# Kernel tuning notes

Hardware: AMD Instinct MI355X
Metric: run time of the kernel (lower is better)

The kernel has to match this reference:

```python
import jax, jax.numpy as jnp
import numpy as np

N_NODES = 100000
N_EDGES = 3200000
IN_CH = 256
OUT_CH = 128


def setup_inputs() -> dict:
    key = jax.random.key(0)
    k1, k2, k3, k4, k5 = jax.random.split(key, 5)
    x = jax.random.normal(k1, (N_NODES, IN_CH), dtype=jnp.float32)
    edge_src = jax.random.randint(k2, (N_EDGES,), 0, N_NODES, dtype=jnp.int64 if jax.config.jax_enable_x64 else jnp.int32)
    edge_dst = jax.random.randint(k3, (N_EDGES,), 0, N_NODES, dtype=jnp.int64 if jax.config.jax_enable_x64 else jnp.int32)
    edge_vals = jax.random.uniform(k4, (N_EDGES,), dtype=jnp.float32)
    weight = jax.random.normal(k5, (IN_CH, OUT_CH), dtype=jnp.float32) * (2.0 / (IN_CH + OUT_CH)) ** 0.5  # glorot
    bias = jnp.zeros((OUT_CH,), dtype=jnp.float32)
    return {"x": x, "edge_src": edge_src, "edge_dst": edge_dst,
            "edge_vals": edge_vals, "weight": weight, "bias": bias}


def reference(x, edge_src, edge_dst, edge_vals, weight, bias):
    # out = A @ (x @ W) + b, with A given in COO form (edge_src=row, edge_dst=col, edge_vals)
    xw = x @ weight                                  # [N, out]
    msgs = xw[edge_dst] * edge_vals[:, None]         # gather source features, scale by edge weight
    agg = jax.ops.segment_sum(msgs, edge_src, num_segments=N_NODES)  # scatter-add to rows
    return agg + bias
```

## Files before the change

kernel.cpp:

```cpp
#include <hip/hip_runtime.h>

#define N_NODES 100000
#define N_EDGES 3200000
#define IN_CH   256
#define OUT_CH  128

#define BSH        5
#define BN         32
#define NBIN       3125
#define NBLK1      256
#define EPB1       12500
#define ITER1      4
#define NS1        (NBIN * NBLK1)
#define SCAN_CHUNK 8192
#define NBLK_S1    ((NS1 + SCAN_CHUNK - 1) / SCAN_CHUNK)
#define SCAP       2048

#define OFF_XWB    0
#define OFF_WBF    25600000
#define OFF_CNTT   25665536
#define OFF_CNTA   28865536
#define OFF_RPA    32065536
#define OFF_RPT    35265552
#define OFF_BS     38465552
#define OFF_RPN    38466576
#define OFF_PACKED 38866592

typedef __attribute__((ext_vector_type(8))) short    bf8;
typedef __attribute__((ext_vector_type(4))) float    f4;
typedef __attribute__((ext_vector_type(4))) unsigned uv4;
typedef __attribute__((ext_vector_type(2))) float    f2v;

__device__ __forceinline__ unsigned f2bf(float f) {
    unsigned u = __float_as_uint(f);
    return (u + 0x7fffu + ((u >> 16) & 1u)) >> 16;
}

__device__ __forceinline__ unsigned cvt_pk_bf16(float lo, float hi) {
    unsigned r;
    asm("v_cvt_pk_bf16_f32 %0, %1, %2" : "=v"(r) : "v"(lo), "v"(hi));
    return r;
}

__global__ __launch_bounds__(256) void wcvt_kernel(const float* __restrict__ w,
                                                   unsigned short* __restrict__ wbf) {
    int t = threadIdx.x;
    int k = blockIdx.x * 2 + (t >> 7);
    int n = t & 127;
    wbf[n * 256 + k] = (unsigned short)f2bf(w[k * 128 + n]);
}

__global__ __launch_bounds__(256) void gemm_kernel(const float* __restrict__ x,
                                                   const unsigned short* __restrict__ wbf,
                                                   unsigned* __restrict__ xwb) {
    int wave = threadIdx.x >> 6;
    int lane = threadIdx.x & 63;
    int m = lane & 15;
    int q = lane >> 4;
    int r0 = blockIdx.x * 64 + wave * 16;

    int arow = r0 + m;
    if (arow >= N_NODES) arow = N_NODES - 1;
    const float* xr = x + (long long)arow * IN_CH + q * 8;

    f4 acc[8];
#pragma unroll
    for (int ct = 0; ct < 8; ++ct) acc[ct] = (f4){0.f, 0.f, 0.f, 0.f};

#pragma unroll
    for (int ks = 0; ks < 8; ++ks) {
        float4 xa = *(const float4*)(xr + ks * 32);
        float4 xb = *(const float4*)(xr + ks * 32 + 4);
        uv4 au;
        au[0] = cvt_pk_bf16(xa.x, xa.y);
        au[1] = cvt_pk_bf16(xa.z, xa.w);
        au[2] = cvt_pk_bf16(xb.x, xb.y);
        au[3] = cvt_pk_bf16(xb.z, xb.w);
        bf8 a = __builtin_bit_cast(bf8, au);
#pragma unroll
        for (int ct = 0; ct < 8; ++ct) {
            uv4 u = *(const uv4*)&wbf[(ct * 16 + m) * 256 + ks * 32 + q * 8];
            bf8 b = __builtin_bit_cast(bf8, u);
            acc[ct] = __builtin_amdgcn_mfma_f32_16x16x32_bf16(a, b, acc[ct], 0, 0, 0);
        }
    }

#pragma unroll
    for (int ct = 0; ct < 8; ++ct) {
#pragma unroll
        for (int r = 0; r < 4; ++r) {
            float v = acc[ct][r];
            float p = __shfl_xor(v, 1, 64);
            unsigned wpk = cvt_pk_bf16(v, p);
            if (!(m & 1)) {
                int row = r0 + q * 4 + r;
                if (row < N_NODES)
                    xwb[row * 64 + ct * 8 + (m >> 1)] = wpk;
            }
        }
    }
}

__global__ __launch_bounds__(1024) void h1_kernel(const int* __restrict__ src,
                                                  int* __restrict__ cntT) {
    __shared__ int lc[NBIN];
    int tid = threadIdx.x;
    int bend = blockIdx.x * EPB1 + EPB1;
    for (int i = tid; i < NBIN; i += 1024) lc[i] = 0;
    __syncthreads();
#pragma unroll
    for (int k = 0; k < ITER1; ++k) {
        int i = blockIdx.x * EPB1 + k * 4096 + tid * 4;
        if (i < bend) {
            int4 s = *(const int4*)&src[i];
            atomicAdd(&lc[s.x >> BSH], 1);
            atomicAdd(&lc[s.y >> BSH], 1);
            atomicAdd(&lc[s.z >> BSH], 1);
            atomicAdd(&lc[s.w >> BSH], 1);
        }
    }
    __syncthreads();
    for (int i = tid; i < NBIN; i += 1024)
        cntT[blockIdx.x * NBIN + i] = lc[i];
}

__global__ __launch_bounds__(256) void transpose_kernel(const int* __restrict__ in,
                                                        int* __restrict__ out,
                                                        int R, int C) {
    __shared__ int t[32][33];
    int tx = threadIdx.x & 31, ty0 = threadIdx.x >> 5;
    int c0 = blockIdx.x * 32, r0 = blockIdx.y * 32;
#pragma unroll
    for (int i = 0; i < 4; ++i) {
        int r = r0 + ty0 + i * 8, c = c0 + tx;
        t[ty0 + i * 8][tx] = (r < R && c < C) ? in[r * C + c] : 0;
    }
    __syncthreads();
#pragma unroll
    for (int i = 0; i < 4; ++i) {
        int c = c0 + ty0 + i * 8, r = r0 + tx;
        if (c < C && r < R) out[c * R + r] = t[tx][ty0 + i * 8];
    }
}

__global__ __launch_bounds__(256) void scan_s1(const int* __restrict__ cnt,
                                               int* __restrict__ bsum) {
    __shared__ int wsum[4];
    int tid = threadIdx.x, lane = tid & 63, wid = tid >> 6;
    int acc = 0;
#pragma unroll
    for (int k = 0; k < SCAN_CHUNK / 1024; ++k) {
        int i0 = blockIdx.x * SCAN_CHUNK + k * 1024 + tid * 4;
        if (i0 < NS1) {
            int4 v = *(const int4*)&cnt[i0];
            acc += v.x + v.y + v.z + v.w;
        }
    }
#pragma unroll
    for (int off = 32; off; off >>= 1) acc += __shfl_down(acc, off, 64);
    if (lane == 0) wsum[wid] = acc;
    __syncthreads();
    if (tid == 0) bsum[blockIdx.x] = wsum[0] + wsum[1] + wsum[2] + wsum[3];
}

__global__ __launch_bounds__(256) void scan_s2(int* __restrict__ bsum,
                                               int* __restrict__ rpA,
                                               int* __restrict__ rpn) {
    __shared__ int wsum[4];
    int tid = threadIdx.x, lane = tid & 63, wid = tid >> 6;
    int v = (tid < NBLK_S1) ? bsum[tid] : 0;
    int s = v;
#pragma unroll
    for (int off = 1; off < 64; off <<= 1) {
        int t = __shfl_up(s, off, 64);
        if (lane >= off) s += t;
    }
    if (lane == 63) wsum[wid] = s;
    __syncthreads();
    int w0 = wsum[0], w1 = wsum[1], w2 = wsum[2], w3 = wsum[3];
    int woff = (wid > 0 ? w0 : 0) + (wid > 1 ? w1 : 0) + (wid > 2 ? w2 : 0);
    if (tid < NBLK_S1) bsum[tid] = woff + s - v;
    if (tid == 0) {
        int tot = w0 + w1 + w2 + w3;
        rpA[NS1] = tot;
        rpn[N_NODES] = tot;
    }
}

__global__ __launch_bounds__(256) void scan_s3(const int* __restrict__ cnt,
                                               const int* __restrict__ bsum,
                                               int* __restrict__ rpA) {
    __shared__ int wsum[4];
    int tid = threadIdx.x, lane = tid & 63, wid = tid >> 6;
    int carry = bsum[blockIdx.x];
#pragma unroll
    for (int k = 0; k < SCAN_CHUNK / 1024; ++k) {
        int i0 = blockIdx.x * SCAN_CHUNK + k * 1024 + tid * 4;
        int4 v = make_int4(0, 0, 0, 0);
        if (i0 < NS1) v = *(const int4*)&cnt[i0];
        int sum4 = v.x + v.y + v.z + v.w;
        int s = sum4;
#pragma unroll
        for (int off = 1; off < 64; off <<= 1) {
            int t = __shfl_up(s, off, 64);
            if (lane >= off) s += t;
        }
        if (lane == 63) wsum[wid] = s;
        __syncthreads();
        int w0 = wsum[0], w1 = wsum[1], w2 = wsum[2], w3 = wsum[3];
        int woff = (wid > 0 ? w0 : 0) + (wid > 1 ? w1 : 0) + (wid > 2 ? w2 : 0);
        int excl = carry + woff + (s - sum4);
        if (i0 < NS1)
            *(int4*)&rpA[i0] = make_int4(excl, excl + v.x, excl + v.x + v.y,
                                         excl + v.x + v.y + v.z);
        carry += w0 + w1 + w2 + w3;
        __syncthreads();
    }
}

__global__ __launch_bounds__(1024) void b1_kernel(const int* __restrict__ src,
                                                  const int* __restrict__ dst,
                                                  const float* __restrict__ val,
                                                  const int* __restrict__ rpT,
                                                  int2* __restrict__ p1) {
    __shared__ int lcur[NBIN];
    int tid = threadIdx.x;
    int bend = blockIdx.x * EPB1 + EPB1;
    for (int i = tid; i < NBIN; i += 1024)
        lcur[i] = rpT[blockIdx.x * NBIN + i];
    __syncthreads();
#pragma unroll
    for (int k = 0; k < ITER1; ++k) {
        int i = blockIdx.x * EPB1 + k * 4096 + tid * 4;
        if (i < bend) {
            int4   s = *(const int4*)&src[i];
            int4   d = *(const int4*)&dst[i];
            float4 v = *(const float4*)&val[i];
            int p;
            p = atomicAdd(&lcur[s.x >> BSH], 1);
            p1[p] = make_int2(d.x | ((s.x & (BN - 1)) << 17), __float_as_int(v.x));
            p = atomicAdd(&lcur[s.y >> BSH], 1);
            p1[p] = make_int2(d.y | ((s.y & (BN - 1)) << 17), __float_as_int(v.y));
            p = atomicAdd(&lcur[s.z >> BSH], 1);
            p1[p] = make_int2(d.z | ((s.z & (BN - 1)) << 17), __float_as_int(v.z));
            p = atomicAdd(&lcur[s.w >> BSH], 1);
            p1[p] = make_int2(d.w | ((s.w & (BN - 1)) << 17), __float_as_int(v.w));
        }
    }
}

__global__ __launch_bounds__(256) void sortf_kernel(const int2* __restrict__ p1,
                                                    const int* __restrict__ rpA,
                                                    int2* __restrict__ packed,
                                                    int* __restrict__ rpn) {
    __shared__ int  lcnt[BN];
    __shared__ int  lcur[BN];
    __shared__ int2 sbuf[SCAP];
    int b = blockIdx.x, tid = threadIdx.x;
    int beg = rpA[b * NBLK1];
    int end = rpA[(b + 1) * NBLK1];
    int n = end - beg;

    if (tid < BN) lcnt[tid] = 0;
    __syncthreads();

    if (n <= SCAP) {
        for (int e = tid; e < n; e += 256) {
            int2 q = p1[beg + e];
            sbuf[e] = q;
            atomicAdd(&lcnt[(q.x >> 17) & (BN - 1)], 1);
        }
    } else {
        for (int e = beg + tid; e < end; e += 256)
            atomicAdd(&lcnt[(p1[e].x >> 17) & (BN - 1)], 1);
    }
    __syncthreads();

    if (tid < BN) {
        int c = lcnt[tid];
        int v = c;
#pragma unroll
        for (int off = 1; off < BN; off <<= 1) {
            int t = __shfl_up(v, off, 64);
            if (tid >= off) v += t;
        }
        int excl = beg + v - c;
        lcur[tid] = excl;
        rpn[b * BN + tid] = excl;
    }
    __syncthreads();

    if (n <= SCAP) {
        for (int e = tid; e < n; e += 256) {
            int2 q = sbuf[e];
            int p = atomicAdd(&lcur[(q.x >> 17) & (BN - 1)], 1);
            packed[p] = make_int2(q.x & 0x1FFFF, q.y);
        }
    } else {
        for (int e = beg + tid; e < end; e += 256) {
            int2 q = p1[e];
            int p = atomicAdd(&lcur[(q.x >> 17) & (BN - 1)], 1);
            packed[p] = make_int2(q.x & 0x1FFFF, q.y);
        }
    }
}

__global__ __launch_bounds__(256) void aggregate_kernel(const int* __restrict__ rp,
                                                        const int2* __restrict__ packed,
                                                        const unsigned* __restrict__ xwb,
                                                        const float* __restrict__ bias,
                                                        float* __restrict__ out) {
    int node = blockIdx.x * 4 + (threadIdx.x >> 6);
    int lane = threadIdx.x & 63;
    float2 bb = *(const float2*)&bias[lane * 2];
    f2v acc; acc[0] = bb.x; acc[1] = bb.y;
    const unsigned* xl = xwb + lane;

    int beg = rp[node];
    int end = rp[node + 1];
    for (int t = beg; t < end; t += 64) {
        int2 rec = make_int2(0, 0);
        if (t + lane < end) rec = packed[t + lane];
        int cnt = end - t; if (cnt > 64) cnt = 64;
        int cntB = (cnt + 15) & ~15;
        for (int j = 0; j < cntB; j += 16) {
            unsigned u[16]; float vv[16];
#pragma unroll
            for (int k = 0; k < 16; ++k) {
                int d  = __builtin_amdgcn_readlane(rec.x, j + k);
                vv[k]  = __int_as_float(__builtin_amdgcn_readlane(rec.y, j + k));
                u[k]   = xl[d * 64];
            }
#pragma unroll
            for (int k = 0; k < 16; ++k) {
                f2v bvec;
                bvec[0] = __uint_as_float(u[k] << 16);
                bvec[1] = __uint_as_float(u[k] & 0xffff0000u);
                acc += vv[k] * bvec;
            }
        }
    }
    float2 o; o.x = acc[0]; o.y = acc[1];
    *(float2*)&out[(long long)node * OUT_CH + lane * 2] = o;
}

extern "C" void kernel_launch(void* const* d_in, const int* in_sizes, int n_in,
                              void* d_out, int out_size, void* d_ws, size_t ws_size,
                              hipStream_t stream) {
    const float* x     = (const float*)d_in[0];
    const int*   esrc  = (const int*)d_in[1];
    const int*   edst  = (const int*)d_in[2];
    const float* evals = (const float*)d_in[3];
    const float* w     = (const float*)d_in[4];
    const float* bias  = (const float*)d_in[5];
    float* out = (float*)d_out;

    char* ws = (char*)d_ws;
    unsigned*       xwb    = (unsigned*)      (ws + OFF_XWB);
    unsigned short* wbf    = (unsigned short*)(ws + OFF_WBF);
    int*            cntT   = (int*)           (ws + OFF_CNTT);
    int*            cntA   = (int*)           (ws + OFF_CNTA);
    int*            rpA    = (int*)           (ws + OFF_RPA);
    int*            rpT    = (int*)           (ws + OFF_RPT);
    int*            bsum   = (int*)           (ws + OFF_BS);
    int*            rpn    = (int*)           (ws + OFF_RPN);
    int2*           packed = (int2*)          (ws + OFF_PACKED);
    int2*           p1     = (int2*)          d_out;

    wcvt_kernel<<<128, 256, 0, stream>>>(w, wbf);
    gemm_kernel<<<(N_NODES + 63) / 64, 256, 0, stream>>>(x, wbf, xwb);
    h1_kernel<<<NBLK1, 1024, 0, stream>>>(esrc, cntT);
    transpose_kernel<<<dim3((NBIN + 31) / 32, (NBLK1 + 31) / 32), 256, 0, stream>>>(
        cntT, cntA, NBLK1, NBIN);
    scan_s1<<<NBLK_S1, 256, 0, stream>>>(cntA, bsum);
    scan_s2<<<1, 256, 0, stream>>>(bsum, rpA, rpn);
    scan_s3<<<NBLK_S1, 256, 0, stream>>>(cntA, bsum, rpA);
    transpose_kernel<<<dim3((NBLK1 + 31) / 32, (NBIN + 31) / 32), 256, 0, stream>>>(
        rpA, rpT, NBIN, NBLK1);
    b1_kernel<<<NBLK1, 1024, 0, stream>>>(esrc, edst, evals, rpT, p1);
    sortf_kernel<<<NBIN, 256, 0, stream>>>(p1, rpA, packed, rpn);
    aggregate_kernel<<<N_NODES / 4, 256, 0, stream>>>(rpn, packed, xwb, bias, out);
}
```

Baseline: 433.6 us.

## Fuse CSR-build pipeline into one cooperative kernel with grid syncs

Replaces the weight conversion, histogram, two transposes, three scan passes, bucket scatter and per-bin sort kernels with a single cooperative kernel of 256 blocks of 1024 threads that separates the phases with grid.sync. This removes about nine kernel launches and the gaps between them. In exchange, the per-bin sort now runs as a grid-stride loop over fewer, larger blocks, and each grid barrier has its own cost. The aggregate kernel is also changed to unroll by 8 instead of 16, and its accumulation moves from packed float2 vector math to scalar float math.

```diff
diff --git a/kernel.cpp b/kernel.cpp
--- a/kernel.cpp
+++ b/kernel.cpp
@@ -1,4 +1,7 @@
 #include <hip/hip_runtime.h>
+#include <hip/hip_cooperative_groups.h>
+
+namespace cg = cooperative_groups;
 
 #define N_NODES 100000
 #define N_EDGES 3200000
@@ -15,6 +18,8 @@
 #define SCAN_CHUNK 8192
 #define NBLK_S1    ((NS1 + SCAN_CHUNK - 1) / SCAN_CHUNK)
 #define SCAP       2048
+#define CBLK       256
+#define CTHR       1024
 
 #define OFF_XWB    0
 #define OFF_WBF    25600000
@@ -29,7 +34,6 @@
 typedef __attribute__((ext_vector_type(8))) short    bf8;
 typedef __attribute__((ext_vector_type(4))) float    f4;
 typedef __attribute__((ext_vector_type(4))) unsigned uv4;
-typedef __attribute__((ext_vector_type(2))) float    f2v;
 
 __device__ __forceinline__ unsigned f2bf(float f) {
     unsigned u = __float_as_uint(f);
@@ -40,14 +44,6 @@
     unsigned r;
     asm("v_cvt_pk_bf16_f32 %0, %1, %2" : "=v"(r) : "v"(lo), "v"(hi));
     return r;
-}
-
-__global__ __launch_bounds__(256) void wcvt_kernel(const float* __restrict__ w,
-                                                   unsigned short* __restrict__ wbf) {
-    int t = threadIdx.x;
-    int k = blockIdx.x * 2 + (t >> 7);
-    int n = t & 127;
-    wbf[n * 256 + k] = (unsigned short)f2bf(w[k * 128 + n]);
 }
 
 __global__ __launch_bounds__(256) void gemm_kernel(const float* __restrict__ x,
@@ -101,207 +97,234 @@
     }
 }
 
-__global__ __launch_bounds__(1024) void h1_kernel(const int* __restrict__ src,
-                                                  int* __restrict__ cntT) {
-    __shared__ int lc[NBIN];
-    int tid = threadIdx.x;
-    int bend = blockIdx.x * EPB1 + EPB1;
-    for (int i = tid; i < NBIN; i += 1024) lc[i] = 0;
+union CoopLds {
+    int lc[NBIN];
+    int tp[32][33];
+    int ws[16];
+    struct { int cnt[BN]; int cur[BN]; int2 buf[SCAP]; } sf;
+};
+
+__global__ __launch_bounds__(1024) void coop_kernel(
+    const float* __restrict__ w,    unsigned short* __restrict__ wbf,
+    const int*   __restrict__ src,  const int* __restrict__ dst,
+    const float* __restrict__ val,
+    int* __restrict__ cntT, int* __restrict__ cntA,
+    int* __restrict__ rpA,  int* __restrict__ rpT,
+    int* __restrict__ bsum, int* __restrict__ rpn,
+    int2* __restrict__ p1,  int2* __restrict__ packed)
+{
+    cg::grid_group grid = cg::this_grid();
+    __shared__ CoopLds S;
+    const int tid  = threadIdx.x;
+    const int b    = blockIdx.x;
+    const int lane = tid & 63;
+    const int wid  = tid >> 6;
+    const int e0   = b * EPB1;
+
+    {
+        int gid = b * CTHR + tid;
+        if (gid < 32768) {
+            int k = gid >> 7, n = gid & 127;
+            wbf[n * 256 + k] = (unsigned short)f2bf(w[k * 128 + n]);
+        }
+    }
+
+    for (int i = tid; i < NBIN; i += CTHR) S.lc[i] = 0;
     __syncthreads();
 #pragma unroll
     for (int k = 0; k < ITER1; ++k) {
-        int i = blockIdx.x * EPB1 + k * 4096 + tid * 4;
-        if (i < bend) {
-            int4 s = *(const int4*)&src[i];
-            atomicAdd(&lc[s.x >> BSH], 1);
-            atomicAdd(&lc[s.y >> BSH], 1);
-            atomicAdd(&lc[s.z >> BSH], 1);
-            atomicAdd(&lc[s.w >> BSH], 1);
+        int i = e0 + k * 4096 + tid * 4;
+        if (i < e0 + EPB1) {
+            int4 s4 = *(const int4*)&src[i];
+            atomicAdd(&S.lc[s4.x >> BSH], 1);
+            atomicAdd(&S.lc[s4.y >> BSH], 1);
+            atomicAdd(&S.lc[s4.z >> BSH], 1);
+            atomicAdd(&S.lc[s4.w >> BSH], 1);
         }
     }
     __syncthreads();
-    for (int i = tid; i < NBIN; i += 1024)
-        cntT[blockIdx.x * NBIN + i] = lc[i];
-}
-
-__global__ __launch_bounds__(256) void transpose_kernel(const int* __restrict__ in,
-                                                        int* __restrict__ out,
-                                                        int R, int C) {
-    __shared__ int t[32][33];
-    int tx = threadIdx.x & 31, ty0 = threadIdx.x >> 5;
-    int c0 = blockIdx.x * 32, r0 = blockIdx.y * 32;
-#pragma unroll
-    for (int i = 0; i < 4; ++i) {
-        int r = r0 + ty0 + i * 8, c = c0 + tx;
-        t[ty0 + i * 8][tx] = (r < R && c < C) ? in[r * C + c] : 0;
-    }
+    for (int i = tid; i < NBIN; i += CTHR) cntT[b * NBIN + i] = S.lc[i];
+    grid.sync();
+
+    {
+        int tx = tid & 31, ty = tid >> 5;
+        for (int t = b; t < 98 * 8; t += CBLK) {
+            int c0 = (t % 98) * 32, r0 = (t / 98) * 32;
+            int r = r0 + ty, c = c0 + tx;
+            S.tp[ty][tx] = (c < NBIN) ? cntT[r * NBIN + c] : 0;
+            __syncthreads();
+            int c2 = c0 + ty, r2 = r0 + tx;
+            if (c2 < NBIN) cntA[c2 * NBLK1 + r2] = S.tp[tx][ty];
+            __syncthreads();
+        }
+    }
+    grid.sync();
+
+    if (b < NBLK_S1) {
+        int acc = 0;
+#pragma unroll
+        for (int k = 0; k < 2; ++k) {
+            int i0 = b * SCAN_CHUNK + k * 4096 + tid * 4;
+            if (i0 < NS1) {
+                int4 v = *(const int4*)&cntA[i0];
+                acc += v.x + v.y + v.z + v.w;
+            }
+        }
+#pragma unroll
+        for (int off = 32; off; off >>= 1) acc += __shfl_down(acc, off, 64);
+        if (lane == 0) S.ws[wid] = acc;
+        __syncthreads();
+        if (tid == 0) {
+            int s = 0;
+            for (int i = 0; i < 16; ++i) s += S.ws[i];
+            bsum[b] = s;
+        }
+    }
+    grid.sync();
+
+    if (b == 0 && wid == 0) {
+        int v0 = (lane < NBLK_S1) ? bsum[lane] : 0;
+        int v1 = (lane + 64 < NBLK_S1) ? bsum[lane + 64] : 0;
+        int s0 = v0;
+#pragma unroll
+        for (int off = 1; off < 64; off <<= 1) {
+            int t2 = __shfl_up(s0, off, 64);
+            if (lane >= off) s0 += t2;
+        }
+        int tot0 = __shfl(s0, 63, 64);
+        int s1 = v1;
+#pragma unroll
+        for (int off = 1; off < 64; off <<= 1) {
+            int t2 = __shfl_up(s1, off, 64);
+            if (lane >= off) s1 += t2;
+        }
+        int tot1 = __shfl(s1, 63, 64);
+        if (lane < NBLK_S1) bsum[lane] = s0 - v0;
+        if (lane + 64 < NBLK_S1) bsum[lane + 64] = tot0 + s1 - v1;
+        if (lane == 0) {
+            rpA[NS1] = tot0 + tot1;
+            rpn[N_NODES] = tot0 + tot1;
+        }
+    }
+    grid.sync();
+
+    if (b < NBLK_S1) {
+        int carry = bsum[b];
+        for (int k = 0; k < 2; ++k) {
+            int i0 = b * SCAN_CHUNK + k * 4096 + tid * 4;
+            int4 v = make_int4(0, 0, 0, 0);
+            if (i0 < NS1) v = *(const int4*)&cntA[i0];
+            int sum4 = v.x + v.y + v.z + v.w;
+            int s = sum4;
+#pragma unroll
+            for (int off = 1; off < 64; off <<= 1) {
+                int t2 = __shfl_up(s, off, 64);
+                if (lane >= off) s += t2;
+            }
+            if (lane == 63) S.ws[wid] = s;
+            __syncthreads();
+            int woff = 0, wtot = 0;
+            for (int i = 0; i < 16; ++i) {
+                int x = S.ws[i];
+                if (i < wid) woff += x;
+                wtot += x;
+            }
+            int excl = carry + woff + (s - sum4);
+            if (i0 < NS1)
+                *(int4*)&rpA[i0] = make_int4(excl, excl + v.x, excl + v.x + v.y,
+                                             excl + v.x + v.y + v.z);
+            carry += wtot;
+            __syncthreads();
+        }
+    }
+    grid.sync();
+
+    {
+        int tx = tid & 31, ty = tid >> 5;
+        for (int t = b; t < 98 * 8; t += CBLK) {
+            int c0 = (t % 8) * 32, r0 = (t / 8) * 32;
+            int r = r0 + ty, c = c0 + tx;
+            S.tp[ty][tx] = (r < NBIN) ? rpA[r * NBLK1 + c] : 0;
+            __syncthreads();
+            int c2 = c0 + ty, r2 = r0 + tx;
+            if (r2 < NBIN) rpT[c2 * NBIN + r2] = S.tp[tx][ty];
+            __syncthreads();
+        }
+    }
+    grid.sync();
+
+    for (int i = tid; i < NBIN; i += CTHR) S.lc[i] = rpT[b * NBIN + i];
     __syncthreads();
 #pragma unroll
-    for (int i = 0; i < 4; ++i) {
-        int c = c0 + ty0 + i * 8, r = r0 + tx;
-        if (c < C && r < R) out[c * R + r] = t[tx][ty0 + i * 8];
-    }
-}
-
-__global__ __launch_bounds__(256) void scan_s1(const int* __restrict__ cnt,
-                                               int* __restrict__ bsum) {
-    __shared__ int wsum[4];
-    int tid = threadIdx.x, lane = tid & 63, wid = tid >> 6;
-    int acc = 0;
-#pragma unroll
-    for (int k = 0; k < SCAN_CHUNK / 1024; ++k) {
-        int i0 = blockIdx.x * SCAN_CHUNK + k * 1024 + tid * 4;
-        if (i0 < NS1) {
-            int4 v = *(const int4*)&cnt[i0];
-            acc += v.x + v.y + v.z + v.w;
-        }
-    }
-#pragma unroll
-    for (int off = 32; off; off >>= 1) acc += __shfl_down(acc, off, 64);
-    if (lane == 0) wsum[wid] = acc;
-    __syncthreads();
-    if (tid == 0) bsum[blockIdx.x] = wsum[0] + wsum[1] + wsum[2] + wsum[3];
-}
-
-__global__ __launch_bounds__(256) void scan_s2(int* __restrict__ bsum,
-                                               int* __restrict__ rpA,
-                                               int* __restrict__ rpn) {
-    __shared__ int wsum[4];
-    int tid = threadIdx.x, lane = tid & 63, wid = tid >> 6;
-    int v = (tid < NBLK_S1) ? bsum[tid] : 0;
-    int s = v;
-#pragma unroll
-    for (int off = 1; off < 64; off <<= 1) {
-        int t = __shfl_up(s, off, 64);
-        if (lane >= off) s += t;
-    }
-    if (lane == 63) wsum[wid] = s;
-    __syncthreads();
-    int w0 = wsum[0], w1 = wsum[1], w2 = wsum[2], w3 = wsum[3];
-    int woff = (wid > 0 ? w0 : 0) + (wid > 1 ? w1 : 0) + (wid > 2 ? w2 : 0);
-    if (tid < NBLK_S1) bsum[tid] = woff + s - v;
-    if (tid == 0) {
-        int tot = w0 + w1 + w2 + w3;
-        rpA[NS1] = tot;
-        rpn[N_NODES] = tot;
-    }
-}
-
-__global__ __launch_bounds__(256) void scan_s3(const int* __restrict__ cnt,
-                                               const int* __restrict__ bsum,
-                                               int* __restrict__ rpA) {
-    __shared__ int wsum[4];
-    int tid = threadIdx.x, lane = tid & 63, wid = tid >> 6;
-    int carry = bsum[blockIdx.x];
-#pragma unroll
-    for (int k = 0; k < SCAN_CHUNK / 1024; ++k) {
-        int i0 = blockIdx.x * SCAN_CHUNK + k * 1024 + tid * 4;
-        int4 v = make_int4(0, 0, 0, 0);
-        if (i0 < NS1) v = *(const int4*)&cnt[i0];
-        int sum4 = v.x + v.y + v.z + v.w;
-        int s = sum4;
-#pragma unroll
-        for (int off = 1; off < 64; off <<= 1) {
-            int t = __shfl_up(s, off, 64);
-            if (lane >= off) s += t;
-        }
-        if (lane == 63) wsum[wid] = s;
-        __syncthreads();
-        int w0 = wsum[0], w1 = wsum[1], w2 = wsum[2], w3 = wsum[3];
-        int woff = (wid > 0 ? w0 : 0) + (wid > 1 ? w1 : 0) + (wid > 2 ? w2 : 0);
-        int excl = carry + woff + (s - sum4);
-        if (i0 < NS1)
-            *(int4*)&rpA[i0] = make_int4(excl, excl + v.x, excl + v.x + v.y,
-                                         excl + v.x + v.y + v.z);
-        carry += w0 + w1 + w2 + w3;
-        __syncthreads();
-    }
-}
-
-__global__ __launch_bounds__(1024) void b1_kernel(const int* __restrict__ src,
-                                                  const int* __restrict__ dst,
-                                                  const float* __restrict__ val,
-                                                  const int* __restrict__ rpT,
-                                                  int2* __restrict__ p1) {
-    __shared__ int lcur[NBIN];
-    int tid = threadIdx.x;
-    int bend = blockIdx.x * EPB1 + EPB1;
-    for (int i = tid; i < NBIN; i += 1024)
-        lcur[i] = rpT[blockIdx.x * NBIN + i];
-    __syncthreads();
-#pragma unroll
     for (int k = 0; k < ITER1; ++k) {
-        int i = blockIdx.x * EPB1 + k * 4096 + tid * 4;
-        if (i < bend) {
-            int4   s = *(const int4*)&src[i];
-            int4   d = *(const int4*)&dst[i];
-            float4 v = *(const float4*)&val[i];
+        int i = e0 + k * 4096 + tid * 4;
+        if (i < e0 + EPB1) {
+            int4   s4 = *(const int4*)&src[i];
+            int4   d4 = *(const int4*)&dst[i];
+            float4 v4 = *(const float4*)&val[i];
             int p;
-            p = atomicAdd(&lcur[s.x >> BSH], 1);
-            p1[p] = make_int2(d.x | ((s.x & (BN - 1)) << 17), __float_as_int(v.x));
-            p = atomicAdd(&lcur[s.y >> BSH], 1);
-            p1[p] = make_int2(d.y | ((s.y & (BN - 1)) << 17), __float_as_int(v.y));
-            p = atomicAdd(&lcur[s.z >> BSH], 1);
-            p1[p] = make_int2(d.z | ((s.z & (BN - 1)) << 17), __float_as_int(v.z));
-            p = atomicAdd(&lcur[s.w >> BSH], 1);
-            p1[p] = make_int2(d.w | ((s.w & (BN - 1)) << 17), __float_as_int(v.w));
-        }
-    }
-}
-
-__global__ __launch_bounds__(256) void sortf_kernel(const int2* __restrict__ p1,
-                                                    const int* __restrict__ rpA,
-                                                    int2* __restrict__ packed,
-                                                    int* __restrict__ rpn) {
-    __shared__ int  lcnt[BN];
-    __shared__ int  lcur[BN];
-    __shared__ int2 sbuf[SCAP];
-    int b = blockIdx.x, tid = threadIdx.x;
-    int beg = rpA[b * NBLK1];
-    int end = rpA[(b + 1) * NBLK1];
-    int n = end - beg;
-
-    if (tid < BN) lcnt[tid] = 0;
-    __syncthreads();
-
-    if (n <= SCAP) {
-        for (int e = tid; e < n; e += 256) {
-            int2 q = p1[beg + e];
-            sbuf[e] = q;
-            atomicAdd(&lcnt[(q.x >> 17) & (BN - 1)], 1);
-        }
-    } else {
-        for (int e = beg + tid; e < end; e += 256)
-            atomicAdd(&lcnt[(p1[e].x >> 17) & (BN - 1)], 1);
-    }
-    __syncthreads();
-
-    if (tid < BN) {
-        int c = lcnt[tid];
-        int v = c;
-#pragma unroll
-        for (int off = 1; off < BN; off <<= 1) {
-            int t = __shfl_up(v, off, 64);
-            if (tid >= off) v += t;
-        }
-        int excl = beg + v - c;
-        lcur[tid] = excl;
-        rpn[b * BN + tid] = excl;
-    }
-    __syncthreads();
-
-    if (n <= SCAP) {
-        for (int e = tid; e < n; e += 256) {
-            int2 q = sbuf[e];
-            int p = atomicAdd(&lcur[(q.x >> 17) & (BN - 1)], 1);
-            packed[p] = make_int2(q.x & 0x1FFFF, q.y);
-        }
-    } else {
-        for (int e = beg + tid; e < end; e += 256) {
-            int2 q = p1[e];
-            int p = atomicAdd(&lcur[(q.x >> 17) & (BN - 1)], 1);
-            packed[p] = make_int2(q.x & 0x1FFFF, q.y);
-        }
+            p = atomicAdd(&S.lc[s4.x >> BSH], 1);
+            p1[p] = make_int2(d4.x | ((s4.x & (BN - 1)) << 17), __float_as_int(v4.x));
+            p = atomicAdd(&S.lc[s4.y >> BSH], 1);
+            p1[p] = make_int2(d4.y | ((s4.y & (BN - 1)) << 17), __float_as_int(v4.y));
+            p = atomicAdd(&S.lc[s4.z >> BSH], 1);
+            p1[p] = make_int2(d4.z | ((s4.z & (BN - 1)) << 17), __float_as_int(v4.z));
+            p = atomicAdd(&S.lc[s4.w >> BSH], 1);
+            p1[p] = make_int2(d4.w | ((s4.w & (BN - 1)) << 17), __float_as_int(v4.w));
+        }
+    }
+    grid.sync();
+
+    for (int bk = b; bk < NBIN; bk += CBLK) {
+        int beg = rpA[bk * NBLK1];
+        int end = rpA[(bk + 1) * NBLK1];
+        int n = end - beg;
+
+        if (tid < BN) S.sf.cnt[tid] = 0;
+        __syncthreads();
+
+        if (n <= SCAP) {
+            for (int e = tid; e < n; e += CTHR) {
+                int2 q = p1[beg + e];
+                S.sf.buf[e] = q;
+                atomicAdd(&S.sf.cnt[(q.x >> 17) & (BN - 1)], 1);
+            }
+        } else {
+            for (int e = beg + tid; e < end; e += CTHR)
+                atomicAdd(&S.sf.cnt[(p1[e].x >> 17) & (BN - 1)], 1);
+        }
+        __syncthreads();
+
+        if (wid == 0) {
+            int c = (lane < BN) ? S.sf.cnt[lane] : 0;
+            int v = c;
+#pragma unroll
+            for (int off = 1; off < BN; off <<= 1) {
+                int t2 = __shfl_up(v, off, 64);
+                if (lane >= off) v += t2;
+            }
+            if (lane < BN) {
+                int excl = beg + v - c;
+                S.sf.cur[lane] = excl;
+                rpn[bk * BN + lane] = excl;
+            }
+        }
+        __syncthreads();
+
+        if (n <= SCAP) {
+            for (int e = tid; e < n; e += CTHR) {
+                int2 q = S.sf.buf[e];
+                int p = atomicAdd(&S.sf.cur[(q.x >> 17) & (BN - 1)], 1);
+                packed[p] = make_int2(q.x & 0x1FFFF, q.y);
+            }
+        } else {
+            for (int e = beg + tid; e < end; e += CTHR) {
+                int2 q = p1[e];
+                int p = atomicAdd(&S.sf.cur[(q.x >> 17) & (BN - 1)], 1);
+                packed[p] = make_int2(q.x & 0x1FFFF, q.y);
+            }
+        }
+        __syncthreads();
     }
 }
 
@@ -312,9 +335,7 @@
                                                         float* __restrict__ out) {
     int node = blockIdx.x * 4 + (threadIdx.x >> 6);
     int lane = threadIdx.x & 63;
-    float2 bb = *(const float2*)&bias[lane * 2];
-    f2v acc; acc[0] = bb.x; acc[1] = bb.y;
-    const unsigned* xl = xwb + lane;
+    float2 acc = *(const float2*)&bias[lane * 2];
 
     int beg = rp[node];
     int end = rp[node + 1];
@@ -322,26 +343,23 @@
         int2 rec = make_int2(0, 0);
         if (t + lane < end) rec = packed[t + lane];
         int cnt = end - t; if (cnt > 64) cnt = 64;
-        int cntB = (cnt + 15) & ~15;
-        for (int j = 0; j < cntB; j += 16) {
-            unsigned u[16]; float vv[16];
-#pragma unroll
-            for (int k = 0; k < 16; ++k) {
+        int cnt8 = (cnt + 7) & ~7;
+        for (int j = 0; j < cnt8; j += 8) {
+            unsigned u[8]; float vv[8];
+#pragma unroll
+            for (int k = 0; k < 8; ++k) {
                 int d  = __builtin_amdgcn_readlane(rec.x, j + k);
                 vv[k]  = __int_as_float(__builtin_amdgcn_readlane(rec.y, j + k));
-                u[k]   = xl[d * 64];
-            }
-#pragma unroll
-            for (int k = 0; k < 16; ++k) {
-                f2v bvec;
-                bvec[0] = __uint_as_float(u[k] << 16);
-                bvec[1] = __uint_as_float(u[k] & 0xffff0000u);
-                acc += vv[k] * bvec;
-            }
-        }
-    }
-    float2 o; o.x = acc[0]; o.y = acc[1];
-    *(float2*)&out[(long long)node * OUT_CH + lane * 2] = o;
+                u[k]   = xwb[d * 64 + lane];
+            }
+#pragma unroll
+            for (int k = 0; k < 8; ++k) {
+                acc.x += vv[k] * __uint_as_float(u[k] << 16);
+                acc.y += vv[k] * __uint_as_float(u[k] & 0xffff0000u);
+            }
+        }
+    }
+    *(float2*)&out[(long long)node * OUT_CH + lane * 2] = acc;
 }
 
 extern "C" void kernel_launch(void* const* d_in, const int* in_sizes, int n_in,
@@ -367,17 +385,12 @@
     int2*           packed = (int2*)          (ws + OFF_PACKED);
     int2*           p1     = (int2*)          d_out;
 
-    wcvt_kernel<<<128, 256, 0, stream>>>(w, wbf);
+    void* cargs[] = { (void*)&w, (void*)&wbf, (void*)&esrc, (void*)&edst,
+                      (void*)&evals, (void*)&cntT, (void*)&cntA, (void*)&rpA,
+                      (void*)&rpT, (void*)&bsum, (void*)&rpn, (void*)&p1,
+                      (void*)&packed };
+    hipLaunchCooperativeKernel((void*)coop_kernel, dim3(CBLK), dim3(CTHR),
+                               cargs, 0, stream);
     gemm_kernel<<<(N_NODES + 63) / 64, 256, 0, stream>>>(x, wbf, xwb);
-    h1_kernel<<<NBLK1, 1024, 0, stream>>>(esrc, cntT);
-    transpose_kernel<<<dim3((NBIN + 31) / 32, (NBLK1 + 31) / 32), 256, 0, stream>>>(
-        cntT, cntA, NBLK1, NBIN);
-    scan_s1<<<NBLK_S1, 256, 0, stream>>>(cntA, bsum);
-    scan_s2<<<1, 256, 0, stream>>>(bsum, rpA, rpn);
-    scan_s3<<<NBLK_S1, 256, 0, stream>>>(cntA, bsum, rpA);
-    transpose_kernel<<<dim3((NBLK1 + 31) / 32, (NBIN + 31) / 32), 256, 0, stream>>>(
-        rpA, rpT, NBIN, NBLK1);
-    b1_kernel<<<NBLK1, 1024, 0, stream>>>(esrc, edst, evals, rpT, p1);
-    sortf_kernel<<<NBIN, 256, 0, stream>>>(p1, rpA, packed, rpn);
     aggregate_kernel<<<N_NODES / 4, 256, 0, stream>>>(rpn, packed, xwb, bias, out);
 }
```

After: 647.8 us. 49.4% more time.
